# Kernel tuning notes

Measured on AMD Instinct MI355X. Metric: run time of the kernel, lower is better.

The kernel has to match this reference:

```python
import jax, jax.numpy as jnp
import numpy as np

VOCAB, EMB, SEQ, HID, TAGS, BATCH = 50000, 300, 256, 256, 50, 128


def _lstm_relu(x, Wx, Wh, b, reverse):
    """Keras LSTM with activation='relu', recurrent_activation='sigmoid'.
    x: [B,S,E] -> returns hidden states [B,S,H]. Gate order i,f,g,o (Keras)."""
    B = x.shape[0]
    H = Wh.shape[0]
    # Precompute input projections for all timesteps: [S,B,4H]
    xz = jnp.einsum('bse,eg->sbg', x, Wx) + b

    def step(carry, z_t):
        h, c = carry
        z = z_t + h @ Wh
        i, f, g, o = jnp.split(z, 4, axis=-1)
        c = jax.nn.sigmoid(f) * c + jax.nn.sigmoid(i) * jax.nn.relu(g)
        h = jax.nn.sigmoid(o) * jax.nn.relu(c)
        return (h, c), h

    h0 = jnp.zeros((B, H), x.dtype)
    _, hs = jax.lax.scan(step, (h0, h0), xz, reverse=reverse)  # hs: [S,B,H] in time order
    return jnp.swapaxes(hs, 0, 1)  # [B,S,H]


def setup_inputs() -> dict:
    key = jax.random.key(0)
    ks = jax.random.split(key, 10)
    s = 0.05  # small init keeps relu-LSTM states numerically tame
    return {
        'tokens': jax.random.randint(ks[0], (BATCH, SEQ), 0, VOCAB, dtype=jnp.int32),
        'emb':    jax.random.normal(ks[1], (VOCAB, EMB), jnp.float32) * s,
        'Wx_f':   jax.random.normal(ks[2], (EMB, 4 * HID), jnp.float32) * s,
        'Wh_f':   jax.random.normal(ks[3], (HID, 4 * HID), jnp.float32) * s,
        'b_f':    jnp.zeros((4 * HID,), jnp.float32),
        'Wx_b':   jax.random.normal(ks[4], (EMB, 4 * HID), jnp.float32) * s,
        'Wh_b':   jax.random.normal(ks[5], (HID, 4 * HID), jnp.float32) * s,
        'b_b':    jnp.zeros((4 * HID,), jnp.float32),
        'Wd':     jax.random.normal(ks[6], (2 * HID, TAGS), jnp.float32) * s,
        'bd':     jnp.zeros((TAGS,), jnp.float32),
    }


def reference(tokens, emb, Wx_f, Wh_f, b_f, Wx_b, Wh_b, b_b, Wd, bd):
    x = emb[tokens]                                  # [B,S,E] embedding lookup
    hf = _lstm_relu(x, Wx_f, Wh_f, b_f, reverse=False)
    hb = _lstm_relu(x, Wx_b, Wh_b, b_b, reverse=True)
    h = jnp.concatenate([hf, hb], axis=-1)           # [B,S,2H]
    # Dropout is identity at inference (Keras default training=False).
    return jax.nn.softmax(h @ Wd + bd, axis=-1)      # [B,S,TAGS]
```

## Files before the change

### kernel.cpp

```cpp
#include <hip/hip_runtime.h>
#include <stdint.h>

#define B_    128
#define S_    256
#define EMB_  300
#define HID_  256
#define TAGS_ 50
#define KPAD  320
#define NROWS (B_ * S_)
#define GF    (4 * HID_)
#define NCOLS (2 * GF)

typedef __bf16 bf16x8 __attribute__((ext_vector_type(8)));
typedef float  f32x4  __attribute__((ext_vector_type(4)));
typedef unsigned int u32x4 __attribute__((ext_vector_type(4)));
typedef int    i32x8  __attribute__((ext_vector_type(8)));

__device__ __forceinline__ unsigned short f2bf(float f) {
    unsigned int u = __float_as_uint(f);
    unsigned int r = (u + 0x7fffu + ((u >> 16) & 1u)) >> 16;
    return (unsigned short)r;
}
__device__ __forceinline__ bf16x8 ldb8(const unsigned short* p) {
    u32x4 v = *reinterpret_cast<const u32x4*>(p);
    return __builtin_bit_cast(bf16x8, v);
}
__device__ __forceinline__ float sigf(float x) {
    return __builtin_amdgcn_rcpf(1.0f + __builtin_amdgcn_exp2f(x * -1.44269504f));
}
__device__ __forceinline__ float sel2(f32x4 v, int p) {
    return p ? v[1] : v[0];
}
__device__ __forceinline__ void gload_lds16(const void* g, void* l) {
    __builtin_amdgcn_global_load_lds(
        (const __attribute__((address_space(1))) void*)g,
        (__attribute__((address_space(3))) void*)l, 16, 0, 0);
}

__global__ void k_gather_x(const int* __restrict__ tokens, const float* __restrict__ emb,
                           unsigned short* __restrict__ X16) {
    int r = blockIdx.x;
    int k = threadIdx.x;
    int b = r & 127, s = r >> 7;
    int tok = tokens[b * S_ + s];
    float v = (k < EMB_) ? emb[(long)tok * EMB_ + k] : 0.0f;
    X16[(long)r * KPAD + k] = f2bf(v);
}

__global__ void k_prep_w(const float* __restrict__ Wx_f, const float* __restrict__ Wx_b,
                         unsigned short* __restrict__ W16T) {
    int c = blockIdx.x;
    int k = threadIdx.x;
    float v = 0.0f;
    if (k < EMB_) v = (c < GF) ? Wx_f[k * GF + c] : Wx_b[k * GF + (c - GF)];
    W16T[c * KPAD + k] = f2bf(v);
}

__global__ void k_prep_wd(const float* __restrict__ Wd, unsigned short* __restrict__ WdT16) {
    int c = blockIdx.x;
    int k = threadIdx.x;
    float v = (c < TAGS_) ? Wd[k * TAGS_ + c] : 0.0f;
    WdT16[c * 512 + k] = f2bf(v);
}

__global__ void k_prep_wh(const float* __restrict__ Wh_f, const float* __restrict__ Wh_b,
                          unsigned short* __restrict__ WhP) {
    int row = blockIdx.x;
    int k = threadIdx.x;
    int d = row >> 10, sl = (row >> 8) & 3, c = row & 255;
    int gate = c >> 6, jrel = c & 63;
    const float* Wh = d ? Wh_b : Wh_f;
    WhP[(long)row * 256 + k] = f2bf(Wh[k * GF + gate * HID_ + sl * 64 + jrel]);
}

__global__ void k_prep_wh8(const float* __restrict__ Wh_f, const float* __restrict__ Wh_b,
                           unsigned char* __restrict__ WhP8) {
    int row = blockIdx.x;
    int k = threadIdx.x;
    int d = row / 768, rr = row - d * 768, gi = rr >> 8, j = rr & 255;
    int ga = (gi == 2) ? 3 : gi;
    const float* Wh = d ? Wh_b : Wh_f;
    float v = Wh[k * GF + ga * HID_ + j];
    int p = __builtin_amdgcn_cvt_pk_fp8_f32(v, 0.0f, 0, false);
    WhP8[(long)row * 256 + k] = (unsigned char)(p & 0xff);
}

__global__ __launch_bounds__(256) void k_gemm_xz(
    const unsigned short* __restrict__ X16, const unsigned short* __restrict__ W16T,
    const float* __restrict__ b_f, const float* __restrict__ b_b,
    unsigned long long* __restrict__ xzP) {
    __shared__ __align__(16) unsigned short Asw[2][128 * 64];
    __shared__ __align__(16) unsigned short Bsw[2][128 * 64];
    int w = threadIdx.x >> 6, lane = threadIdx.x & 63;
    int quad = lane >> 4, l16 = lane & 15;
    int m0 = blockIdx.x * 128;
    int n0 = blockIdx.y * 128;

    int rlane = lane >> 3;
    int jpos  = lane & 7;
    int jsrc  = jpos ^ (rlane & 7);

    f32x4 acc[2][8];
#pragma unroll
    for (int mt = 0; mt < 2; ++mt)
#pragma unroll
        for (int nt = 0; nt < 8; ++nt) acc[mt][nt] = (f32x4){0.f, 0.f, 0.f, 0.f};

#define STAGE(ST, BUFI) do {                                                    \
    int k0_ = (ST) * 64;                                                        \
    _Pragma("unroll")                                                           \
    for (int i_ = 0; i_ < 4; ++i_) {                                            \
        int rb_ = (w * 4 + i_) * 8;                                             \
        int r_  = rb_ + rlane;                                                  \
        gload_lds16(X16 + (long)(m0 + r_) * KPAD + k0_ + jsrc * 8,              \
                    &Asw[BUFI][rb_ * 64]);                                      \
    }                                                                           \
    _Pragma("unroll")                                                           \
    for (int i_ = 0; i_ < 4; ++i_) {                                            \
        int rb_ = (w * 4 + i_) * 8;                                             \
        int r_  = rb_ + rlane;                                                  \
        gload_lds16(W16T + (long)(n0 + r_) * KPAD + k0_ + jsrc * 8,             \
                    &Bsw[BUFI][rb_ * 64]);                                      \
    }                                                                           \
} while (0)

    STAGE(0, 0);
    __syncthreads();
#pragma unroll
    for (int st = 0; st < 5; ++st) {
        if (st < 4) STAGE(st + 1, (st + 1) & 1);
        int bufi = st & 1;
#pragma unroll
        for (int ks = 0; ks < 2; ++ks) {
            bf16x8 a[2], bb[8];
#pragma unroll
            for (int mt = 0; mt < 2; ++mt) {
                int mrow = w * 32 + mt * 16 + l16;
                int jp = (ks * 4 + quad) ^ (l16 & 7);
                a[mt] = ldb8(&Asw[bufi][mrow * 64 + jp * 8]);
            }
#pragma unroll
            for (int nt = 0; nt < 8; ++nt) {
                int nrow = nt * 16 + l16;
                int jp = (ks * 4 + quad) ^ (l16 & 7);
                bb[nt] = ldb8(&Bsw[bufi][nrow * 64 + jp * 8]);
            }
#pragma unroll
            for (int mt = 0; mt < 2; ++mt)
#pragma unroll
                for (int nt = 0; nt < 8; ++nt)
                    acc[mt][nt] = __builtin_amdgcn_mfma_f32_16x16x32_bf16(a[mt], bb[nt], acc[mt][nt], 0, 0, 0);
        }
        __syncthreads();
    }
#undef STAGE

    int s = blockIdx.x;
#pragma unroll
    for (int mt = 0; mt < 2; ++mt) {
        int grp = w * 2 + mt;
#pragma unroll
        for (int nt = 0; nt < 8; ++nt) {
            int col = n0 + nt * 16 + l16;
            int dir = col >> 10, cc = col & 1023;
            int gate = cc >> 8, u16 = (cc & 255) >> 4;
            float bias = dir ? b_b[cc] : b_f[cc];
            unsigned long long pk = 0;
#pragma unroll
            for (int r = 0; r < 4; ++r)
                pk |= (unsigned long long)f2bf(acc[mt][nt][r] + bias) << (16 * r);
            long idx8 = ((long)(s * 16 + dir * 8 + grp)) * 4096 +
                        (gate * 16 + u16) * 64 + quad * 16 + l16;
            xzP[idx8] = pk;
        }
    }
}

__global__ __launch_bounds__(512, 2) void k_recurrence(
    const unsigned short* __restrict__ WhP, const unsigned char* __restrict__ WhP8,
    const unsigned long long* __restrict__ xzP, unsigned short* __restrict__ hcat16) {
    __shared__ __align__(16) unsigned char lds[3328];
    const int HB = 0, H8 = 2176;
    int tid = threadIdx.x;
    int w = tid >> 6, lane = tid & 63, quad = lane >> 4, l16 = lane & 15;
    int blk = blockIdx.x;
    int d = blk >> 6, bg2 = blk & 63;
    int p = quad & 1;
    int cg = quad >> 1;
    int col = 16 * (2 * w + cg) + l16;
    int rp = l16 & 1;

    u32x4 whg[2][8];
#pragma unroll
    for (int cgi = 0; cgi < 2; ++cgi) {
        int j = 16 * (2 * w + cgi) + l16;
        int sl = j >> 6, jrel = j & 63;
        const unsigned short* src = WhP + ((long)((d * 4 + sl) * 256 + 128 + jrel)) * 256;
#pragma unroll
        for (int kt = 0; kt < 8; ++kt) {
            u32x4 v = *reinterpret_cast<const u32x4*>(src + kt * 32 + quad * 8);
            asm volatile("" : "+v"(v));
            whg[cgi][kt] = v;
        }
    }
    i32x8 wh8s[3][2][2];
#pragma unroll
    for (int gi = 0; gi < 3; ++gi)
#pragma unroll
        for (int cgi = 0; cgi < 2; ++cgi)
#pragma unroll
            for (int kt2 = 0; kt2 < 2; ++kt2) {
                const unsigned char* wp8 = WhP8 +
                    ((long)((d * 3 + gi) * 256 + 16 * (2 * w + cgi) + l16)) * 256 +
                    kt2 * 128 + quad * 32;
                i32x8 v = *reinterpret_cast<const i32x8*>(wp8);
                asm volatile("" : "+v"(v));
                wh8s[gi][cgi][kt2] = v;
            }

    float c2 = 0.f;

    const unsigned short* xzU = (const unsigned short*)xzP;
    int rowc = d * 8 + (bg2 >> 3);
    unsigned int laneoff = (unsigned)((2 * w + cg) * 256 +
                                      (((bg2 >> 1) & 3) * 16 + l16) * 4 +
                                      2 * (bg2 & 1) + p);

    unsigned short xzu[4];
    {
        int s0 = d ? 255 : 0;
        const unsigned short* ps = xzU + (unsigned long)(s0 * 16 + rowc) * 16384;
#pragma unroll
        for (int ga = 0; ga < 4; ++ga) xzu[ga] = ps[laneoff + ga * 4096];
    }

    for (int t = 0; t < 256; ++t) {
        int s = d ? (255 - t) : t;
        int pb = t & 1, cb = pb ^ 1;
        f32x4 accg[2];
        f32x4 acc8[3][2];
#pragma unroll
        for (int cgi = 0; cgi < 2; ++cgi) {
            accg[cgi] = (f32x4){0.f, 0.f, 0.f, 0.f};
#pragma unroll
            for (int gi = 0; gi < 3; ++gi) acc8[gi][cgi] = (f32x4){0.f, 0.f, 0.f, 0.f};
        }

        if (t > 0) {
#pragma unroll
            for (int kt = 0; kt < 8; ++kt) {
                bf16x8 A = ldb8(reinterpret_cast<const unsigned short*>(
                    lds + HB + cb * 1088 + rp * 544 + kt * 64 + quad * 16));
#pragma unroll
                for (int cgi = 0; cgi < 2; ++cgi)
                    accg[cgi] = __builtin_amdgcn_mfma_f32_16x16x32_bf16(
                        A, __builtin_bit_cast(bf16x8, whg[cgi][kt]), accg[cgi], 0, 0, 0);
            }
#pragma unroll
            for (int kt2 = 0; kt2 < 2; ++kt2) {
                i32x8 A8 = *reinterpret_cast<const i32x8*>(
                    lds + H8 + cb * 576 + rp * 288 + kt2 * 128 + quad * 32);
#pragma unroll
                for (int cgi = 0; cgi < 2; ++cgi)
#pragma unroll
                    for (int gi = 0; gi < 3; ++gi)
#if __has_builtin(__builtin_amdgcn_mfma_scale_f32_16x16x128_f8f6f4)
                        acc8[gi][cgi] = __builtin_amdgcn_mfma_scale_f32_16x16x128_f8f6f4(
                            A8, wh8s[gi][cgi][kt2], acc8[gi][cgi], 0, 0, 0, 0x7F, 0, 0x7F);
#else
                        acc8[gi][cgi] = acc8[gi][cgi];
#endif
            }
        }
        float xa0 = __uint_as_float((unsigned int)xzu[0] << 16);
        float xa1 = __uint_as_float((unsigned int)xzu[1] << 16);
        float xa2 = __uint_as_float((unsigned int)xzu[2] << 16);
        float xa3 = __uint_as_float((unsigned int)xzu[3] << 16);
        {
            int sn = d ? (s ? s - 1 : 0) : (s < 255 ? s + 1 : 255);
            const unsigned short* ps = xzU + (unsigned long)(sn * 16 + rowc) * 16384;
#pragma unroll
            for (int ga = 0; ga < 4; ++ga) xzu[ga] = ps[laneoff + ga * 4096];
        }
        float zi = (cg ? sel2(acc8[0][1], p) : sel2(acc8[0][0], p)) + xa0;
        float zf = (cg ? sel2(acc8[1][1], p) : sel2(acc8[1][0], p)) + xa1;
        float zg = (cg ? sel2(accg[1],    p) : sel2(accg[0],    p)) + xa2;
        float zo = (cg ? sel2(acc8[2][1], p) : sel2(acc8[2][0], p)) + xa3;
        float c = sigf(zf) * c2 + sigf(zi) * fmaxf(zg, 0.0f);
        c2 = c;
        float h = sigf(zo) * fmaxf(c, 0.0f);

        unsigned short hb16 = f2bf(h);
        *reinterpret_cast<unsigned short*>(lds + HB + pb * 1088 + p * 544 + col * 2) = hb16;
        int p8 = __builtin_amdgcn_cvt_pk_fp8_f32(h, h, 0, false);
        *(lds + H8 + pb * 576 + p * 288 + col) = (unsigned char)(p8 & 0xff);
        hcat16[((long)(bg2 * 2 + p) * S_ + s) * 512 + d * HID_ + col] = hb16;
        asm volatile("s_waitcnt lgkmcnt(0)\n\ts_barrier" ::: "memory");
    }
}

__global__ __launch_bounds__(256) void k_gemm_logits(
    const unsigned short* __restrict__ hcat16, const unsigned short* __restrict__ WdT16,
    float* __restrict__ logits) {
    int w = threadIdx.x >> 6, lane = threadIdx.x & 63;
    int quad = lane >> 4, l16 = lane & 15;
    int m0 = blockIdx.x * 128 + w * 32;
    f32x4 acc[2][4];
#pragma unroll
    for (int mt = 0; mt < 2; ++mt)
#pragma unroll
        for (int nt = 0; nt < 4; ++nt) acc[mt][nt] = (f32x4){0.f, 0.f, 0.f, 0.f};
#pragma unroll
    for (int ks = 0; ks < 16; ++ks) {
        int k0 = ks * 32 + quad * 8;
        bf16x8 a[2], bb[4];
#pragma unroll
        for (int mt = 0; mt < 2; ++mt)
            a[mt] = ldb8(hcat16 + (long)(m0 + mt * 16 + l16) * 512 + k0);
#pragma unroll
        for (int nt = 0; nt < 4; ++nt)
            bb[nt] = ldb8(WdT16 + (long)(nt * 16 + l16) * 512 + k0);
#pragma unroll
        for (int mt = 0; mt < 2; ++mt)
#pragma unroll
            for (int nt = 0; nt < 4; ++nt)
                acc[mt][nt] = __builtin_amdgcn_mfma_f32_16x16x32_bf16(a[mt], bb[nt], acc[mt][nt], 0, 0, 0);
    }
#pragma unroll
    for (int mt = 0; mt < 2; ++mt)
#pragma unroll
        for (int nt = 0; nt < 4; ++nt) {
            int rbase = m0 + mt * 16 + quad * 4;
            int col = nt * 16 + l16;
#pragma unroll
            for (int r = 0; r < 4; ++r)
                logits[(long)(rbase + r) * 64 + col] = acc[mt][nt][r];
        }
}

__global__ __launch_bounds__(256) void k_softmax(const float* __restrict__ logits,
                                                 const float* __restrict__ bd,
                                                 float* __restrict__ out) {
    int w = threadIdx.x >> 6, lane = threadIdx.x & 63;
    long r = (long)blockIdx.x * 4 + w;
    float x = (lane < TAGS_) ? logits[r * 64 + lane] + bd[lane] : -3.0e38f;
    float m = x;
#pragma unroll
    for (int off = 32; off >= 1; off >>= 1) m = fmaxf(m, __shfl_xor(m, off, 64));
    float e = (lane < TAGS_) ? __expf(x - m) : 0.0f;
    float ssum = e;
#pragma unroll
    for (int off = 32; off >= 1; off >>= 1) ssum += __shfl_xor(ssum, off, 64);
    if (lane < TAGS_) out[r * TAGS_ + lane] = e / ssum;
}

extern "C" void kernel_launch(void* const* d_in, const int* in_sizes, int n_in,
                              void* d_out, int out_size, void* d_ws, size_t ws_size,
                              hipStream_t stream) {
    (void)in_sizes; (void)n_in; (void)out_size; (void)ws_size;
    const int*   tokens = (const int*)  d_in[0];
    const float* emb    = (const float*)d_in[1];
    const float* Wx_f   = (const float*)d_in[2];
    const float* Wh_f   = (const float*)d_in[3];
    const float* b_f    = (const float*)d_in[4];
    const float* Wx_b   = (const float*)d_in[5];
    const float* Wh_b   = (const float*)d_in[6];
    const float* b_b    = (const float*)d_in[7];
    const float* Wd     = (const float*)d_in[8];
    const float* bd     = (const float*)d_in[9];
    float* out = (float*)d_out;

    uint8_t* w = (uint8_t*)d_ws;
    unsigned short* X16    = (unsigned short*)(w);
    unsigned short* WhP    = (unsigned short*)(w);
    unsigned char*  WhP8   = (unsigned char*)(w + 1048576);
    unsigned short* W16T   = (unsigned short*)(w + 20971520);
    unsigned short* WdT16  = (unsigned short*)(w + 22282240);
    unsigned long long* xzP = (unsigned long long*)(w + 22347776);
    unsigned short* hcat16 = (unsigned short*)(w + 156565504);
    float*          logits = (float*)(w + 22347776);

    k_gather_x  <<<dim3(NROWS),     dim3(KPAD), 0, stream>>>(tokens, emb, X16);
    k_prep_w    <<<dim3(NCOLS),     dim3(KPAD), 0, stream>>>(Wx_f, Wx_b, W16T);
    k_prep_wd   <<<dim3(64),        dim3(512),  0, stream>>>(Wd, WdT16);
    k_gemm_xz   <<<dim3(256, 16),   dim3(256),  0, stream>>>(X16, W16T, b_f, b_b, xzP);
    k_prep_wh   <<<dim3(2048),      dim3(256),  0, stream>>>(Wh_f, Wh_b, WhP);
    k_prep_wh8  <<<dim3(1536),      dim3(256),  0, stream>>>(Wh_f, Wh_b, WhP8);
    k_recurrence<<<dim3(128),       dim3(512),  0, stream>>>(WhP, WhP8, xzP, hcat16);
    k_gemm_logits<<<dim3(256),      dim3(256),  0, stream>>>(hcat16, WdT16, logits);
    k_softmax   <<<dim3(NROWS / 4), dim3(256),  0, stream>>>(logits, bd, out);
}
```

Measured before the change: 456.3 us.

## Move g-gate recurrence to FP8 MFMA and fuse softmax into logits GEMM

The recurrent matmul for the g gate previously used bf16 MFMA (8 k-steps) while the other gates used FP8. Now all four gates use FP8 weights and FP8 hidden state via the scaled 16x16x128 MFMA. This drops the bf16 weight prep kernel and the bf16 LDS hidden buffer, shortening the serial per-step critical path. Separately, softmax with bias is computed in the logits GEMM epilogue using 16-lane shuffles, removing the logits round-trip and one launch. The cost is lower precision on the g gate, so accuracy may suffer.

```diff
diff --git a/kernel.cpp b/kernel.cpp
--- a/kernel.cpp
+++ b/kernel.cpp
@@ -63,24 +63,13 @@
     WdT16[c * 512 + k] = f2bf(v);
 }
 
-__global__ void k_prep_wh(const float* __restrict__ Wh_f, const float* __restrict__ Wh_b,
-                          unsigned short* __restrict__ WhP) {
-    int row = blockIdx.x;
-    int k = threadIdx.x;
-    int d = row >> 10, sl = (row >> 8) & 3, c = row & 255;
-    int gate = c >> 6, jrel = c & 63;
-    const float* Wh = d ? Wh_b : Wh_f;
-    WhP[(long)row * 256 + k] = f2bf(Wh[k * GF + gate * HID_ + sl * 64 + jrel]);
-}
-
 __global__ void k_prep_wh8(const float* __restrict__ Wh_f, const float* __restrict__ Wh_b,
                            unsigned char* __restrict__ WhP8) {
     int row = blockIdx.x;
     int k = threadIdx.x;
-    int d = row / 768, rr = row - d * 768, gi = rr >> 8, j = rr & 255;
-    int ga = (gi == 2) ? 3 : gi;
+    int d = row >> 10, rr = row & 1023, gi = rr >> 8, j = rr & 255;
     const float* Wh = d ? Wh_b : Wh_f;
-    float v = Wh[k * GF + ga * HID_ + j];
+    float v = Wh[k * GF + gi * HID_ + j];
     int p = __builtin_amdgcn_cvt_pk_fp8_f32(v, 0.0f, 0, false);
     WhP8[(long)row * 256 + k] = (unsigned char)(p & 0xff);
 }
@@ -177,10 +166,9 @@
 }
 
 __global__ __launch_bounds__(512, 2) void k_recurrence(
-    const unsigned short* __restrict__ WhP, const unsigned char* __restrict__ WhP8,
+    const unsigned char* __restrict__ WhP8,
     const unsigned long long* __restrict__ xzP, unsigned short* __restrict__ hcat16) {
-    __shared__ __align__(16) unsigned char lds[3328];
-    const int HB = 0, H8 = 2176;
+    __shared__ __align__(16) unsigned char lds[1152];
     int tid = threadIdx.x;
     int w = tid >> 6, lane = tid & 63, quad = lane >> 4, l16 = lane & 15;
     int blk = blockIdx.x;
@@ -190,28 +178,15 @@
     int col = 16 * (2 * w + cg) + l16;
     int rp = l16 & 1;
 
-    u32x4 whg[2][8];
-#pragma unroll
-    for (int cgi = 0; cgi < 2; ++cgi) {
-        int j = 16 * (2 * w + cgi) + l16;
-        int sl = j >> 6, jrel = j & 63;
-        const unsigned short* src = WhP + ((long)((d * 4 + sl) * 256 + 128 + jrel)) * 256;
-#pragma unroll
-        for (int kt = 0; kt < 8; ++kt) {
-            u32x4 v = *reinterpret_cast<const u32x4*>(src + kt * 32 + quad * 8);
-            asm volatile("" : "+v"(v));
-            whg[cgi][kt] = v;
-        }
-    }
-    i32x8 wh8s[3][2][2];
-#pragma unroll
-    for (int gi = 0; gi < 3; ++gi)
+    i32x8 wh8s[4][2][2];
+#pragma unroll
+    for (int gi = 0; gi < 4; ++gi)
 #pragma unroll
         for (int cgi = 0; cgi < 2; ++cgi)
 #pragma unroll
             for (int kt2 = 0; kt2 < 2; ++kt2) {
                 const unsigned char* wp8 = WhP8 +
-                    ((long)((d * 3 + gi) * 256 + 16 * (2 * w + cgi) + l16)) * 256 +
+                    ((long)((d * 4 + gi) * 256 + 16 * (2 * w + cgi) + l16)) * 256 +
                     kt2 * 128 + quad * 32;
                 i32x8 v = *reinterpret_cast<const i32x8*>(wp8);
                 asm volatile("" : "+v"(v));
@@ -237,33 +212,21 @@
     for (int t = 0; t < 256; ++t) {
         int s = d ? (255 - t) : t;
         int pb = t & 1, cb = pb ^ 1;
-        f32x4 accg[2];
-        f32x4 acc8[3][2];
-#pragma unroll
-        for (int cgi = 0; cgi < 2; ++cgi) {
-            accg[cgi] = (f32x4){0.f, 0.f, 0.f, 0.f};
-#pragma unroll
-            for (int gi = 0; gi < 3; ++gi) acc8[gi][cgi] = (f32x4){0.f, 0.f, 0.f, 0.f};
-        }
+        f32x4 acc8[4][2];
+#pragma unroll
+        for (int gi = 0; gi < 4; ++gi)
+#pragma unroll
+            for (int cgi = 0; cgi < 2; ++cgi) acc8[gi][cgi] = (f32x4){0.f, 0.f, 0.f, 0.f};
 
         if (t > 0) {
-#pragma unroll
-            for (int kt = 0; kt < 8; ++kt) {
-                bf16x8 A = ldb8(reinterpret_cast<const unsigned short*>(
-                    lds + HB + cb * 1088 + rp * 544 + kt * 64 + quad * 16));
-#pragma unroll
-                for (int cgi = 0; cgi < 2; ++cgi)
-                    accg[cgi] = __builtin_amdgcn_mfma_f32_16x16x32_bf16(
-                        A, __builtin_bit_cast(bf16x8, whg[cgi][kt]), accg[cgi], 0, 0, 0);
-            }
 #pragma unroll
             for (int kt2 = 0; kt2 < 2; ++kt2) {
                 i32x8 A8 = *reinterpret_cast<const i32x8*>(
-                    lds + H8 + cb * 576 + rp * 288 + kt2 * 128 + quad * 32);
+                    lds + cb * 576 + rp * 288 + kt2 * 128 + quad * 32);
 #pragma unroll
                 for (int cgi = 0; cgi < 2; ++cgi)
 #pragma unroll
-                    for (int gi = 0; gi < 3; ++gi)
+                    for (int gi = 0; gi < 4; ++gi)
 #if __has_builtin(__builtin_amdgcn_mfma_scale_f32_16x16x128_f8f6f4)
                         acc8[gi][cgi] = __builtin_amdgcn_mfma_scale_f32_16x16x128_f8f6f4(
                             A8, wh8s[gi][cgi][kt2], acc8[gi][cgi], 0, 0, 0, 0x7F, 0, 0x7F);
@@ -284,24 +247,22 @@
         }
         float zi = (cg ? sel2(acc8[0][1], p) : sel2(acc8[0][0], p)) + xa0;
         float zf = (cg ? sel2(acc8[1][1], p) : sel2(acc8[1][0], p)) + xa1;
-        float zg = (cg ? sel2(accg[1],    p) : sel2(accg[0],    p)) + xa2;
-        float zo = (cg ? sel2(acc8[2][1], p) : sel2(acc8[2][0], p)) + xa3;
+        float zg = (cg ? sel2(acc8[2][1], p) : sel2(acc8[2][0], p)) + xa2;
+        float zo = (cg ? sel2(acc8[3][1], p) : sel2(acc8[3][0], p)) + xa3;
         float c = sigf(zf) * c2 + sigf(zi) * fmaxf(zg, 0.0f);
         c2 = c;
         float h = sigf(zo) * fmaxf(c, 0.0f);
 
-        unsigned short hb16 = f2bf(h);
-        *reinterpret_cast<unsigned short*>(lds + HB + pb * 1088 + p * 544 + col * 2) = hb16;
         int p8 = __builtin_amdgcn_cvt_pk_fp8_f32(h, h, 0, false);
-        *(lds + H8 + pb * 576 + p * 288 + col) = (unsigned char)(p8 & 0xff);
-        hcat16[((long)(bg2 * 2 + p) * S_ + s) * 512 + d * HID_ + col] = hb16;
+        *(lds + pb * 576 + p * 288 + col) = (unsigned char)(p8 & 0xff);
+        hcat16[((long)(bg2 * 2 + p) * S_ + s) * 512 + d * HID_ + col] = f2bf(h);
         asm volatile("s_waitcnt lgkmcnt(0)\n\ts_barrier" ::: "memory");
     }
 }
 
 __global__ __launch_bounds__(256) void k_gemm_logits(
     const unsigned short* __restrict__ hcat16, const unsigned short* __restrict__ WdT16,
-    float* __restrict__ logits) {
+    const float* __restrict__ bd, float* __restrict__ out) {
     int w = threadIdx.x >> 6, lane = threadIdx.x & 63;
     int quad = lane >> 4, l16 = lane & 15;
     int m0 = blockIdx.x * 128 + w * 32;
@@ -327,31 +288,39 @@
                 acc[mt][nt] = __builtin_amdgcn_mfma_f32_16x16x32_bf16(a[mt], bb[nt], acc[mt][nt], 0, 0, 0);
     }
 #pragma unroll
-    for (int mt = 0; mt < 2; ++mt)
-#pragma unroll
-        for (int nt = 0; nt < 4; ++nt) {
-            int rbase = m0 + mt * 16 + quad * 4;
-            int col = nt * 16 + l16;
-#pragma unroll
-            for (int r = 0; r < 4; ++r)
-                logits[(long)(rbase + r) * 64 + col] = acc[mt][nt][r];
-        }
-}
-
-__global__ __launch_bounds__(256) void k_softmax(const float* __restrict__ logits,
-                                                 const float* __restrict__ bd,
-                                                 float* __restrict__ out) {
-    int w = threadIdx.x >> 6, lane = threadIdx.x & 63;
-    long r = (long)blockIdx.x * 4 + w;
-    float x = (lane < TAGS_) ? logits[r * 64 + lane] + bd[lane] : -3.0e38f;
-    float m = x;
-#pragma unroll
-    for (int off = 32; off >= 1; off >>= 1) m = fmaxf(m, __shfl_xor(m, off, 64));
-    float e = (lane < TAGS_) ? __expf(x - m) : 0.0f;
-    float ssum = e;
-#pragma unroll
-    for (int off = 32; off >= 1; off >>= 1) ssum += __shfl_xor(ssum, off, 64);
-    if (lane < TAGS_) out[r * TAGS_ + lane] = e / ssum;
+    for (int mt = 0; mt < 2; ++mt) {
+#pragma unroll
+        for (int r = 0; r < 4; ++r) {
+            int row = m0 + mt * 16 + quad * 4 + r;
+            float vv[4];
+            float mx = -3.0e38f;
+#pragma unroll
+            for (int nt = 0; nt < 4; ++nt) {
+                int cl = nt * 16 + l16;
+                float tv = (cl < TAGS_) ? (acc[mt][nt][r] + bd[cl]) : -3.0e38f;
+                vv[nt] = tv;
+                mx = fmaxf(mx, tv);
+            }
+#pragma unroll
+            for (int off = 8; off >= 1; off >>= 1) mx = fmaxf(mx, __shfl_xor(mx, off, 64));
+            float sum = 0.f;
+#pragma unroll
+            for (int nt = 0; nt < 4; ++nt) {
+                int cl = nt * 16 + l16;
+                float e = (cl < TAGS_) ? __expf(vv[nt] - mx) : 0.0f;
+                vv[nt] = e;
+                sum += e;
+            }
+#pragma unroll
+            for (int off = 8; off >= 1; off >>= 1) sum += __shfl_xor(sum, off, 64);
+            float rs = __builtin_amdgcn_rcpf(sum);
+#pragma unroll
+            for (int nt = 0; nt < 4; ++nt) {
+                int cl = nt * 16 + l16;
+                if (cl < TAGS_) out[(long)row * TAGS_ + cl] = vv[nt] * rs;
+            }
+        }
+    }
 }
 
 extern "C" void kernel_launch(void* const* d_in, const int* in_sizes, int n_in,
@@ -372,21 +341,17 @@
 
     uint8_t* w = (uint8_t*)d_ws;
     unsigned short* X16    = (unsigned short*)(w);
-    unsigned short* WhP    = (unsigned short*)(w);
-    unsigned char*  WhP8   = (unsigned char*)(w + 1048576);
+    unsigned char*  WhP8   = (unsigned char*)(w);
     unsigned short* W16T   = (unsigned short*)(w + 20971520);
     unsigned short* WdT16  = (unsigned short*)(w + 22282240);
     unsigned long long* xzP = (unsigned long long*)(w + 22347776);
     unsigned short* hcat16 = (unsigned short*)(w + 156565504);
-    float*          logits = (float*)(w + 22347776);
 
     k_gather_x  <<<dim3(NROWS),     dim3(KPAD), 0, stream>>>(tokens, emb, X16);
     k_prep_w    <<<dim3(NCOLS),     dim3(KPAD), 0, stream>>>(Wx_f, Wx_b, W16T);
     k_prep_wd   <<<dim3(64),        dim3(512),  0, stream>>>(Wd, WdT16);
     k_gemm_xz   <<<dim3(256, 16),   dim3(256),  0, stream>>>(X16, W16T, b_f, b_b, xzP);
-    k_prep_wh   <<<dim3(2048),      dim3(256),  0, stream>>>(Wh_f, Wh_b, WhP);
-    k_prep_wh8  <<<dim3(1536),      dim3(256),  0, stream>>>(Wh_f, Wh_b, WhP8);
-    k_recurrence<<<dim3(128),       dim3(512),  0, stream>>>(WhP, WhP8, xzP, hcat16);
-    k_gemm_logits<<<dim3(256),      dim3(256),  0, stream>>>(hcat16, WdT16, logits);
-    k_softmax   <<<dim3(NROWS / 4), dim3(256),  0, stream>>>(logits, bd, out);
-}
+    k_prep_wh8  <<<dim3(2048),      dim3(256),  0, stream>>>(Wh_f, Wh_b, WhP8);
+    k_recurrence<<<dim3(128),       dim3(512),  0, stream>>>(WhP8, xzP, hcat16);
+    k_gemm_logits<<<dim3(256),      dim3(256),  0, stream>>>(hcat16, WdT16, bd, out);
+}
```

Measured after the change: 423.0 us. 7.3% less time.
